# Performance work log

Hardware: AMD Instinct MI355X
Metric: run time of the kernel (lower is better)

## Reference

```python
import jax, jax.numpy as jnp
import numpy as np
from jax import lax

B, T, C, H, W = 2, 5, 2, 128, 256
E, M, L = 64, 16, 4  # embedding_dim, n_fno_modes, n_fno_layers
EPS = 1e-5


def conv1x1(x, w, b):
    # x: [N, I, H, W], w: [O, I], b: [O]
    return jnp.einsum('nihw,oi->nohw', x, w) + b[None, :, None, None]


def conv3x3(x, w, b):
    # x: [N, I, H, W], w: [O, I, 3, 3]
    y = lax.conv_general_dilated(x, w, window_strides=(1, 1), padding='SAME',
                                 dimension_numbers=('NCHW', 'OIHW', 'NCHW'))
    return y + b[None, :, None, None]


def instance_norm(x):
    # InstanceNorm2d(affine=False): normalize over H,W per (n, c), biased var
    mu = jnp.mean(x, axis=(2, 3), keepdims=True)
    var = jnp.var(x, axis=(2, 3), keepdims=True)
    return (x - mu) * lax.rsqrt(var + EPS)


def upsample2x_nearest(x):
    return jnp.repeat(jnp.repeat(x, 2, axis=2), 2, axis=3)


def resize_nearest(x, out_h, out_w):
    # torch F.interpolate mode='nearest': idx = floor(i * in / out)
    in_h, in_w = x.shape[2], x.shape[3]
    hi = (jnp.arange(out_h) * in_h) // out_h
    wi = (jnp.arange(out_w) * in_w) // out_w
    return x[:, :, hi, :][:, :, :, wi]


def fno_layer(x, wr, wi, cw, cb):
    # x: [N, E, H, W]; wr/wi: [2, E, E, M, M]; cw: [E, E]; cb: [E]
    h, w = x.shape[2], x.shape[3]
    coeff = jnp.fft.rfft2(x, axes=(2, 3), norm='ortho')  # [N, E, H, W//2+1]
    w0 = wr[0] + 1j * wi[0]
    w1 = wr[1] + 1j * wi[1]
    out = jnp.zeros_like(coeff)
    out = out.at[:, :, :M, :M].set(
        jnp.einsum('nixy,ioxy->noxy', coeff[:, :, :M, :M], w0))
    out = out.at[:, :, -M:, :M].set(
        jnp.einsum('nixy,ioxy->noxy', coeff[:, :, -M:, :M], w1))
    spec = jnp.fft.irfft2(out, s=(h, w), axes=(2, 3), norm='ortho')
    return jax.nn.gelu(conv1x1(x, cw, cb) + spec, approximate=False)


def setup_inputs() -> dict:
    key = jax.random.key(0)
    ks = jax.random.split(key, 10)
    s = 0.02
    return {
        'sensor_value': jax.random.normal(ks[0], (B, T, C, H, W), jnp.float32),
        'updim_w': 0.3 * jax.random.normal(ks[1], (E, C), jnp.float32),
        'updim_b': jnp.zeros((E,), jnp.float32),
        'smooth_w': 0.04 * jax.random.normal(ks[2], (E, E, 3, 3), jnp.float32),
        'smooth_b': jnp.zeros((E,), jnp.float32),
        'fno_wr': s * jax.random.normal(ks[3], (L, 2, E, E, M, M), jnp.float32),
        'fno_wi': s * jax.random.normal(ks[4], (L, 2, E, E, M, M), jnp.float32),
        'fno_cw': 0.1 * jax.random.normal(ks[5], (L, E, E), jnp.float32),
        'fno_cb': jnp.zeros((L, E), jnp.float32),
        'downdim_w': 0.1 * jax.random.normal(ks[6], (C, E), jnp.float32),
        'downdim_b': jnp.zeros((C,), jnp.float32),
    }


def reference(sensor_value, updim_w, updim_b, smooth_w, smooth_b,
              fno_wr, fno_wi, fno_cw, fno_cb, downdim_w, downdim_b):
    b, t, c, h, w = sensor_value.shape
    x = sensor_value.reshape(b * t, c, h, w)
    x = conv1x1(x, updim_w, updim_b)
    x = upsample2x_nearest(x)
    x = jax.nn.gelu(instance_norm(conv3x3(x, smooth_w, smooth_b)), approximate=False)
    x = resize_nearest(x, H, W)
    for l in range(L):
        x = fno_layer(x, fno_wr[l], fno_wi[l], fno_cw[l], fno_cb[l])
    x = conv1x1(x, downdim_w, downdim_b)
    return x.reshape(b, t, c, H, W)
```

## Files before the change

kernel.cpp:

```cpp
#include <hip/hip_runtime.h>
#include <math.h>

#define PI_D 3.14159265358979323846


typedef _Float16 h8 __attribute__((ext_vector_type(8)));
typedef float f16v __attribute__((ext_vector_type(16)));

__device__ __forceinline__ float gelu_f(float v){
  return 0.5f*v*(1.0f + erff(v*0.70710678118654752440f));
}

__device__ __forceinline__ int fsw_c(int w){ return (w ^ (w >> 3)) & 7; }

__global__ __launch_bounds__(256) void k_tables_fold(float* __restrict__ twFwH, float* __restrict__ twBwH,
                                                     _Float16* __restrict__ Tspec, _Float16* __restrict__ TdftW,
                                                     const float* __restrict__ smw, const float* __restrict__ upw,
                                                     const float* __restrict__ upb, float* __restrict__ Keff){
  int bid = blockIdx.x;
  if (bid < 96){
    int id = bid*256 + threadIdx.x;
    if (id < 4096){
      int h = id >> 5, m = id & 31;
      int xm = (m < 16) ? m : (96 + m);
      double ang = -2.0*PI_D*(double)((xm*h) & 127)/128.0;
      twFwH[id*2]   = (float)cos(ang);
      twFwH[id*2+1] = (float)sin(ang);
    } else if (id < 8192){
      int j = id - 4096;
      int h = j >> 5, m = j & 31;
      int xm = (m < 16) ? m : (96 + m);
      double ang = 2.0*PI_D*(double)((xm*h) & 127)/128.0;
      twBwH[j*2]   = (float)cos(ang);
      twBwH[j*2+1] = (float)sin(ang);
    } else if (id < 16384){
      int j = id - 8192;
      int w = j >> 5, kk = j & 31;
      int y = kk >> 1;
      double ang = 2.0*PI_D*(double)((w*y) & 255)/256.0;
      double v = (kk & 1) ? -sin(ang) : cos(ang);
      Tspec[j] = (_Float16)v;
    } else if (id < 24576){
      int j = id - 16384;
      int y2 = j >> 8, w = j & 255;
      int y = y2 >> 1;
      double ang = -2.0*PI_D*(double)((w*y) & 255)/256.0;
      double v = (y2 & 1) ? sin(ang) : cos(ang);
      TdftW[j] = (_Float16)v;
    }
  } else {
    int id = (bid-96)*256 + threadIdx.x;
    if (id >= 1024) return;
    int o = id >> 4, rs = (id >> 2) & 3, tap = id & 3;
    int r = rs >> 1, s = rs & 1, a = tap >> 1, b = tap & 1;
    int klo = (r==0) ? (a==0?0:1) : (a==0?0:2);
    int khi = (r==0) ? (a==0?0:2) : (a==0?1:2);
    int llo = (s==0) ? (b==0?0:1) : (b==0?0:2);
    int lhi = (s==0) ? (b==0?0:2) : (b==0?1:2);
    float a0=0.f, a1=0.f, ab=0.f;
    for (int i=0;i<64;++i){
      float t = 0.f;
      for (int kh=klo; kh<=khi; ++kh)
        for (int kw=llo; kw<=lhi; ++kw)
          t += smw[((size_t)o*64+i)*9 + kh*3+kw];
      a0 += t*upw[i*2];
      a1 += t*upw[i*2+1];
      ab += t*upb[i];
    }
    *(float4*)(Keff + o*64 + (rs*4+tap)*4) = make_float4(a0, a1, ab, 0.f);
  }
}

__global__ __launch_bounds__(256) void k_transW(const float* __restrict__ wr, const float* __restrict__ wi,
                                                unsigned* __restrict__ Wt){
  __shared__ unsigned P[64*257];
  int lb = blockIdx.x;
  int i = lb & 63, blk = (lb>>6)&1, l = lb>>7;
  int tid = threadIdx.x;
  size_t sbase = (size_t)l*2097152 + (size_t)blk*1048576 + (size_t)i*16384 + tid;
  for (int o=0;o<64;++o){
    float a = wr[sbase + (size_t)o*256];
    float b = wi[sbase + (size_t)o*256];
    union { unsigned u; _Float16 h[2]; } pk;
    pk.h[0] = (_Float16)a; pk.h[1] = (_Float16)b;
    P[o*257 + tid] = pk.u;
  }
  __syncthreads();
  int o = tid & 63, g = tid >> 6;
  size_t dbase = (size_t)(l*2+blk)*1048576;
  for (int it=0; it<64; ++it){
    int my = g*64 + it;
    Wt[dbase + (size_t)my*4096 + i*64 + o] = P[o*257 + my];
  }
}

__global__ __launch_bounds__(512) void k_corrbnd(const float* __restrict__ sv, float* __restrict__ Rpart,
                                                 float* __restrict__ Bnd){
  __shared__ float SH[3120];
  int bid = blockIdx.x;
  int tid = threadIdx.x;
  if (bid < 320){
    int band = bid & 31, n = bid >> 5;
    int u0 = band*4;
    for (int t = tid; t < 3120; t += 512){
      int ch = t / 1560; int rem = t - ch*1560; int rr = rem / 260; int ci = rem - rr*260;
      int row = u0 - 1 + rr, col = ci - 1;
      float v = 0.f;
      if (row >= 0 && row < 128 && col >= 0 && col < 256)
        v = sv[((size_t)(n*2+ch)*128 + row)*256 + col];
      SH[(ch*6+rr)*260 + ci] = v;
    }
    __syncthreads();

    int lane = tid & 63, wv = tid >> 6;
    int c  = (wv<4) ? (wv>>1) : ((wv<6) ? (wv-4) : 2);
    int c2 = (wv<4) ? (wv&1)  : ((wv<6) ? 2 : (wv-6));
    float acc[9];
    #pragma unroll
    for (int k=0;k<9;++k) acc[k]=0.f;

    for (int r=0;r<4;++r){
      int u = u0 + r, lu = r + 1;
      for (int cb=0;cb<4;++cb){
        int v = cb*64 + lane;
        float f = (c==2) ? 1.f : SH[(c*6+lu)*260 + 1+v];
        #pragma unroll
        for (int dr=-1;dr<=1;++dr){
          int ur = u + dr;
          float rko = (ur>=0 && ur<128) ? 1.f : 0.f;
          #pragma unroll
          for (int dc=-1;dc<=1;++dc){
            float g;
            if (c2==2){
              int vc = v + dc;
              g = rko * ((vc>=0 && vc<256) ? 1.f : 0.f);
            } else {
              g = SH[(c2*6+lu+dr)*260 + 1+v+dc];
            }
            acc[(dr+1)*3 + dc+1] += f*g;
          }
        }
      }
    }
    #pragma unroll
    for (int k=0;k<9;++k){
      float v = acc[k];
      for (int off=32; off; off>>=1) v += __shfl_xor(v, off);
      if (lane==0) Rpart[((size_t)(n*32+band)*8 + wv)*9 + k] = v;
    }
  } else {
    int n = bid - 320;
    for (int t = tid; t < 3120; t += 512){
      int e = t/780; int rem = t - e*780; int ch = rem/260; int i = rem - ch*260;
      int idx = i - 1;
      int len = (e<2) ? 256 : 128;
      float v = 0.f;
      if (idx >= 0 && idx < len){
        if (ch==2) v = 1.f;
        else {
          int row = (e==0) ? 0 : (e==1) ? 127 : idx;
          int col = (e==2) ? 0 : (e==3) ? 255 : idx;
          v = sv[((size_t)(n*2+ch)*128 + row)*256 + col];
        }
      }
      SH[(e*3+ch)*260 + i] = v;
    }
    __syncthreads();
    if (tid < 108){
      int e = tid/27; int rem = tid - e*27; int pair = rem/3; int lag = rem%3 - 1;
      int c = pair/3, c2 = pair%3;
      int len = (e<2) ? 256 : 128;
      float a = 0.f;
      for (int i=0;i<len;++i) a += SH[(e*3+c)*260 + 1+i]*SH[(e*3+c2)*260 + 1+i+lag];
      Bnd[n*144 + tid] = a;
    } else if (tid < 144){
      int t = tid - 108; int corner = t/9; int pair = t - corner*9;
      int c = pair/3, c2 = pair%3;
      int e = (corner<2) ? 0 : 1;
      int idx = (corner&1) ? 255 : 0;
      Bnd[n*144 + tid] = SH[(e*3+c)*260 + 1+idx]*SH[(e*3+c2)*260 + 1+idx];
    }
  }
}

__global__ __launch_bounds__(256) void k_stats3(const float* __restrict__ Rpart, const float* __restrict__ Bnd,
                                                const float* __restrict__ Keff, float* __restrict__ stats){
  __shared__ float R[9][9];
  __shared__ float BL[4][9][3];
  __shared__ float CR[4][9];
  __shared__ float M[4][12][12];
  int n = blockIdx.x, tid = threadIdx.x;

  if (tid < 72){
    int wv = tid/9, k = tid - (tid/9)*9;
    double s = 0.0;
    for (int b=0;b<32;++b) s += (double)Rpart[((size_t)(n*32+b)*8 + wv)*9 + k];
    int c  = (wv<4) ? (wv>>1) : ((wv<6) ? (wv-4) : 2);
    int c2 = (wv<4) ? (wv&1)  : ((wv<6) ? 2 : (wv-6));
    R[c*3+c2][k] = (float)s;
  } else if (tid < 81){
    int k = tid - 72; int dr = k/3 - 1, dc = k%3 - 1;
    R[8][k] = (float)((128 - (dr<0?-dr:dr)) * (256 - (dc<0?-dc:dc)));
  }
  if (tid < 108){
    int e = tid/27, rem = tid - (tid/27)*27;
    BL[e][rem/3][rem%3] = Bnd[n*144 + tid];
  } else if (tid < 144){
    int t = tid - 108;
    CR[t/9][t - (t/9)*9] = Bnd[n*144 + tid];
  }
  __syncthreads();

  for (int t = tid; t < 576; t += 256){
    int rs = t/144; int rem = t - rs*144; int i = rem/12, j = rem - (rem/12)*12;
    int ab = i/3,  c  = i - ab*3,  a  = ab>>1, b  = ab&1;
    int ab2 = j/3, c2 = j - ab2*3, a2 = ab2>>1, b2 = ab2&1;
    int r = rs>>1, s = rs&1;
    int dr = a2 - a, dc = b2 - b;
    int pair = c*3 + c2;
    float g = R[pair][(dr+1)*3 + (dc+1)];
    if (r==1 && a==1 && a2==1) g -= BL[0][pair][dc+1];
    if (r==0 && a==0 && a2==0) g -= BL[1][pair][dc+1];
    if (s==1 && b==1 && b2==1) g -= BL[2][pair][dr+1];
    if (s==0 && b==0 && b2==0) g -= BL[3][pair][dr+1];
    bool rowc = (a==a2) && ((r==1 && a==1) || (r==0 && a==0));
    bool colc = (b==b2) && ((s==1 && b==1) || (s==0 && b==0));
    if (rowc && colc){
      int corner = ((r==1)?0:2) + ((s==1)?0:1);
      g += CR[corner][pair];
    }
    M[rs][i][j] = g;
  }
  __syncthreads();

  if (tid < 64){
    int o = tid;
    double S1 = 0.0, S2 = 0.0;
    for (int rs=0; rs<4; ++rs){
      float w[12];
      #pragma unroll
      for (int ab=0; ab<4; ++ab){
        float4 kv = *(const float4*)(Keff + o*64 + (rs*4+ab)*4);
        w[ab*3+0] = kv.x; w[ab*3+1] = kv.y; w[ab*3+2] = kv.z;
      }
      #pragma unroll
      for (int i=0;i<12;++i){
        double ti = 0.0;
        #pragma unroll
        for (int j=0;j<12;++j) ti += (double)M[rs][i][j]*(double)w[j];
        S2 += (double)w[i]*ti;
      }
      #pragma unroll
      for (int ab=0; ab<4; ++ab)
        #pragma unroll
        for (int c=0;c<3;++c)
          S1 += (double)w[ab*3+c]*(double)M[rs][ab*3+c][ab*3+2];
    }
    double mu  = S1 / 131072.0;
    double var = S2 / 131072.0 - mu*mu;
    stats[(n*64+o)*2]   = (float)mu;
    stats[(n*64+o)*2+1] = (float)(1.0/sqrt(var + 1e-5));
  }
}

__global__ __launch_bounds__(256) void k_convnorm(const float* __restrict__ sv,
                                                  const float* __restrict__ Keff,
                                                  const float* __restrict__ stats,
                                                  _Float16* __restrict__ act){
  __shared__ float SV[4*260];
  int bid = blockIdx.x;
  int p = bid & 127, n = bid >> 7;
  int tid = threadIdx.x;
  for (int t = tid; t < 1032; t += 256){
    int dr = t / 516;
    int rem = t - dr*516;
    int ch = rem / 258;
    int ci = rem - ch*258;
    int row = p - 1 + dr;
    int col = ci - 1;
    float v = 0.f;
    if (row >= 0 && col >= 0 && col < 256)
      v = sv[((size_t)(n*2+ch)*128 + row)*256 + col];
    SV[(dr*2+ch)*260 + ci] = v;
  }
  __syncthreads();

  int q = tid;
  float x0[4], x1[4], ib[4];
  float rowok0 = (p>0)?1.f:0.f;
  float colok0 = (q>0)?1.f:0.f;
  #pragma unroll
  for (int a=0;a<2;++a)
    #pragma unroll
    for (int b=0;b<2;++b){
      x0[a*2+b] = SV[(a*2+0)*260 + q + b];
      x1[a*2+b] = SV[(a*2+1)*260 + q + b];
      ib[a*2+b] = (a==0?rowok0:1.f) * (b==0?colok0:1.f);
    }

  for (int o=0; o<64; ++o){
    const float4* kp = (const float4*)(Keff + o*64);
    float y = 0.f;
    #pragma unroll
    for (int t=0;t<4;++t){
      float4 kv = kp[t];
      y += kv.x*x0[t] + kv.y*x1[t] + kv.z*ib[t];
    }
    float mu = stats[(n*64+o)*2], istd = stats[(n*64+o)*2+1];
    float v = (y - mu)*istd;
    act[((size_t)(n*64+o)*128 + p)*256 + q] = (_Float16)gelu_f(v);
  }
}

__global__ __launch_bounds__(256, 2) void k_dftW_mfma(const _Float16* __restrict__ act,
                                                      const _Float16* __restrict__ TdftW,
                                                      float* __restrict__ Cy){
  __shared__ _Float16 Ax[32768];
  __shared__ _Float16 Bt[8192];
  int tid = threadIdx.x;
  int hp = blockIdx.x & 63, n = blockIdx.x >> 6;
  int h0 = hp*2;

  {
    int a = tid >> 1;
    int ws = (tid & 1) * 128;
    int e = a & 63, ht = a >> 6;
    const _Float16* src = act + ((size_t)(n*64+e))*32768 + (size_t)(h0+ht)*256 + ws;
    #pragma unroll
    for (int k=0;k<16;++k){
      h8 v = *(const h8*)(src + k*8);
      int wq = (ws >> 3) + k;
      int chunk = wq ^ (a & 7);
      *(h8*)(Ax + a*256 + chunk*8) = v;
    }
  }
  {
    int y2 = tid & 31, ws = (tid >> 5) * 32;
    const _Float16* src = TdftW + y2*256 + ws;
    #pragma unroll
    for (int k=0;k<4;++k){
      h8 v = *(const h8*)(src + k*8);
      int wq = (ws >> 3) + k;
      int chunk = wq ^ (y2 & 7);
      *(h8*)(Bt + y2*256 + chunk*8) = v;
    }
  }
  __syncthreads();

  int lane = tid & 63;
  int l31 = lane & 31, l5 = lane >> 5;
  int mt = tid >> 6;
  int a = mt*32 + l31;

  f16v acc;
  #pragma unroll
  for (int j=0;j<16;++j) acc[j] = 0.f;
  #pragma unroll
  for (int ks=0;ks<16;++ks){
    int kb = ks*16 + l5*8;
    int cA = (kb>>3) ^ (a & 7);
    int cB = (kb>>3) ^ (l31 & 7);
    h8 af = *(const h8*)(Ax + a*256 + cA*8);
    h8 bf = *(const h8*)(Bt + l31*256 + cB*8);
    acc = __builtin_amdgcn_mfma_f32_32x32x16_f16(bf, af, acc, 0,0,0);
  }
  int e = a & 63, ht = a >> 6;
  #pragma unroll
  for (int j=0;j<16;j+=2){
    int y2 = (j&3) + 8*(j>>2) + 4*l5;
    int yy = y2 >> 1;
    *(float2*)(Cy + (((size_t)(n*16+yy)*128 + h0+ht)*64 + e)*2) = make_float2(acc[j], acc[j+1]);
  }
}

__global__ __launch_bounds__(256) void k_specAB(const float* __restrict__ Cy,
                                                const float* __restrict__ twF,
                                                const unsigned* __restrict__ Wt,
                                                float* __restrict__ MS, int l){
  __shared__ float CO[8*64*2];
  int bid = blockIdx.x;
  int mq = bid / 160;
  int pid = bid - mq*160;
  int y = pid & 15, n = pid >> 4;
  int tid = threadIdx.x;
  int lane = tid & 63;
  int wv = __builtin_amdgcn_readfirstlane(tid >> 6);

  {
    int m0 = mq*8 + wv*2;
    const float* cyb = Cy + (((size_t)(n*16+y)*128)*64 + lane)*2;
    const float* tf = twF + m0*2;
    float ar0=0.f, ai0=0.f, ar1=0.f, ai1=0.f;
    for (int h=0; h<128; ++h){
      float2 c = *(const float2*)(cyb + h*128);
      const float* tp = tf + h*64;
      float t0r = tp[0], t0i = tp[1], t1r = tp[2], t1i = tp[3];
      ar0 += t0r*c.x - t0i*c.y; ai0 += t0r*c.y + t0i*c.x;
      ar1 += t1r*c.x - t1i*c.y; ai1 += t1r*c.y + t1i*c.x;
    }
    int mm = wv*2;
    *(float2*)(CO + (mm*64 + lane)*2)     = make_float2(ar0, ai0);
    *(float2*)(CO + ((mm+1)*64 + lane)*2) = make_float2(ar1, ai1);
  }
  __syncthreads();

  {
    #pragma unroll
    for (int t2=0; t2<2; ++t2){
      int mm = wv*2 + t2;
      int m = mq*8 + mm;
      int blk = m >> 4, mloc = m & 15;
      int my = mloc*16 + y;
      const unsigned* wb = Wt + ((size_t)((l*2+blk)*256 + my))*4096 + lane;
      float mr = 0.f, mi = 0.f;
      for (int i=0;i<64;++i){
        float2 cc = *(const float2*)(CO + (mm*64 + i)*2);
        union { unsigned u; _Float16 h[2]; } pk;
        pk.u = wb[(size_t)i*64];
        float wr_f = (float)pk.h[0], wi_f = (float)pk.h[1];
        mr += cc.x*wr_f - cc.y*wi_f;
        mi += cc.x*wi_f + cc.y*wr_f;
      }
      *(float2*)(MS + (((size_t)(n*16+y)*32 + m)*64 + lane)*2) = make_float2(mr, mi);
    }
  }
}

__global__ __launch_bounds__(256) void k_specC(const float* __restrict__ MS,
                                               const float* __restrict__ twB,
                                               float* __restrict__ G){
  __shared__ float SM[32*64*2];
  int bid = blockIdx.x;
  int hq = bid / 160;
  int pid = bid - hq*160;
  int y = pid & 15, n = pid >> 4;
  int tid = threadIdx.x;
  int lane = tid & 63;
  int wv = __builtin_amdgcn_readfirstlane(tid >> 6);

  {
    const float4* src = (const float4*)(MS + ((size_t)(n*16+y)*32)*128);
    float4* dst = (float4*)SM;
    #pragma unroll
    for (int t=0; t<4; ++t) dst[tid + t*256] = src[tid + t*256];
  }
  __syncthreads();

  float f = (y==0) ? (1.f/32768.f) : (2.f/32768.f);
  for (int k=0;k<8;++k){
    int h = hq*32 + wv*8 + k;
    const float* tb = twB + h*64;
    float gr=0.f, gi=0.f;
    #pragma unroll
    for (int m=0;m<32;++m){
      float tr = tb[m*2], ti = tb[m*2+1];
      float2 mo2 = *(const float2*)(SM + (m*64+lane)*2);
      gr += tr*mo2.x - ti*mo2.y;
      gi += tr*mo2.y + ti*mo2.x;
    }
    size_t gb = (((size_t)(n*128+h)*16 + y)*2)*64 + lane;
    G[gb]      = gr*f;
    G[gb + 64] = gi*f;
  }
}

__global__ __launch_bounds__(512, 4) void k_combine_mfma(const _Float16* __restrict__ act_in,
                                                         const float* __restrict__ G,
                                                         const _Float16* __restrict__ Tspec,
                                                         const _Float16* __restrict__ TdftW,
                                                         const float* __restrict__ cw,
                                                         const float* __restrict__ cb,
                                                         const float* __restrict__ wd,
                                                         const float* __restrict__ bd,
                                                         _Float16* __restrict__ act_out,
                                                         float* __restrict__ Cy,
                                                         float* __restrict__ outp,
                                                         int flags){
  __shared__ __align__(16) _Float16 Lh[40960];
  _Float16* Bx = Lh;
  _Float16* At = Lh + 32768;
  int tid = threadIdx.x;
  int h = blockIdx.x & 127, n = blockIdx.x >> 7;

  {
    int rp = tid >> 4, sub = tid & 15;
    int i0 = 2*rp;
    int wbase = sub*16;
    const _Float16* r0 = act_in + (size_t)(n*64+i0)*32768 + (size_t)h*256 + wbase;
    const _Float16* r1 = r0 + 32768;
    h8 A0 = *(const h8*)r0,     A1 = *(const h8*)(r0+8);
    h8 B0 = *(const h8*)r1,     B1 = *(const h8*)(r1+8);
    int cbs = rp >> 2;
    int lo  = i0 & 7;
    #pragma unroll
    for (int k=0;k<16;++k){
      union { _Float16 hh[2]; unsigned u; } pk;
      pk.hh[0] = (k<8) ? A0[k] : A1[k-8];
      pk.hh[1] = (k<8) ? B0[k] : B1[k-8];
      int w = wbase + k;
      int chunk = cbs ^ fsw_c(w);
      *(unsigned*)(Bx + w*128 + chunk*8 + lo) = pk.u;
    }
  }
  {
    int o = tid >> 3, seg = (tid & 7)*8;
    float4 c0 = *(const float4*)(cw + o*64 + seg);
    float4 c1 = *(const float4*)(cw + o*64 + seg + 4);
    h8 v;
    v[0]=(_Float16)c0.x; v[1]=(_Float16)c0.y; v[2]=(_Float16)c0.z; v[3]=(_Float16)c0.w;
    v[4]=(_Float16)c1.x; v[5]=(_Float16)c1.y; v[6]=(_Float16)c1.z; v[7]=(_Float16)c1.w;
    int ch0 = (seg>>3) ^ (o & 7);
    *(h8*)(At + o*128 + ch0*8) = v;
  }
  {
    const float* gp = G + (size_t)(n*128 + h)*2048 + tid*4;
    float4 g = *(const float4*)gp;
    float gvx[4] = {g.x, g.y, g.z, g.w};
    int idx0 = tid*4;
    int yc = idx0 >> 6;
    int o0 = idx0 & 63;
    int kk = 64 + yc;
    #pragma unroll
    for (int j=0;j<4;++j){
      int o = o0 + j;
      int chunk = (kk >> 3) ^ (o & 7);
      At[o*128 + chunk*8 + (kk & 7)] = (_Float16)gvx[j];
    }
  }
  {
    int w = tid >> 1, half = tid & 1;
    const _Float16* tp = Tspec + w*32 + half*16;
    #pragma unroll
    for (int c=0;c<2;++c){
      h8 v = *(const h8*)(tp + c*8);
      int cc = half*2 + c;
      int chunk = (8 + cc) ^ fsw_c(w);
      *(h8*)(Bx + w*128 + chunk*8) = v;
    }
  }
  __syncthreads();

  int lane = tid & 63;
  int l31 = lane & 31, l5 = lane >> 5;
  int w0i = tid >> 6;
  int mt = w0i & 1, ng = w0i >> 1;
  int o_lane = mt*32 + l31;

  h8 af[6];
  #pragma unroll
  for (int ks=0;ks<6;++ks){
    int kb = ks*16 + l5*8;
    int chunk = (kb>>3) ^ (o_lane & 7);
    af[ks] = *(const h8*)(At + o_lane*128 + chunk*8);
  }
  float bias[16];
  #pragma unroll
  for (int j=0;j<16;++j) bias[j] = cb[mt*32 + (j&3) + 8*(j>>2) + 4*l5];

  f16v acc[2];
  #pragma unroll
  for (int q=0;q<2;++q)
    #pragma unroll
    for (int j=0;j<16;++j) acc[q][j] = bias[j];

  #pragma unroll
  for (int q=0;q<2;++q){
    int w = (ng*2+q)*32 + l31;
    const _Float16* bbase = Bx + w*128;
    int wf = fsw_c(w);
    #pragma unroll
    for (int ks=0;ks<6;++ks){
      int kb = ks*16 + l5*8;
      int chunk = (kb>>3) ^ wf;
      h8 bf = *(const h8*)(bbase + chunk*8);
      acc[q] = __builtin_amdgcn_mfma_f32_32x32x16_f16(af[ks], bf, acc[q], 0,0,0);
    }
  }

  float gvv[32];
  #pragma unroll
  for (int q=0;q<2;++q)
    #pragma unroll
    for (int j=0;j<16;++j) gvv[q*16+j] = gelu_f(acc[q][j]);

  if (flags != 2){
    #pragma unroll
    for (int q=0;q<2;++q){
      int wcol = (ng*2+q)*32 + l31;
      #pragma unroll
      for (int j=0;j<16;++j){
        int o = mt*32 + (j&3) + 8*(j>>2) + 4*l5;
        act_out[(size_t)(n*64+o)*32768 + (size_t)h*256 + wcol] = (_Float16)gvv[q*16+j];
      }
    }
  }
  __syncthreads();

  if (flags == 1){
    _Float16* gL  = Lh;
    _Float16* TdL = Lh + 16384;
    #pragma unroll
    for (int q=0;q<2;++q){
      int wcol = (ng*2+q)*32 + l31;
      int wc3 = wcol >> 3, wc7 = wcol & 7;
      #pragma unroll
      for (int j=0;j<16;++j){
        int o = mt*32 + (j&3) + 8*(j>>2) + 4*l5;
        gL[o*256 + ((wc3 ^ (o & 7))*8) + wc7] = (_Float16)gvv[q*16+j];
      }
    }
    {
      int y2 = tid & 31, ws = (tid >> 5)*16;
      const _Float16* src = TdftW + y2*256 + ws;
      #pragma unroll
      for (int k=0;k<2;++k){
        h8 v = *(const h8*)(src + k*8);
        int chunk = ((ws>>3)+k) ^ (y2 & 7);
        *(h8*)(TdL + y2*256 + chunk*8) = v;
      }
    }
    __syncthreads();
    float* P = (float*)(Lh + 32768);
    if (w0i < 4){
      int mt2 = w0i & 1, kh = w0i >> 1;
      int ocol = mt2*32 + l31;
      f16v acc2;
      #pragma unroll
      for (int j=0;j<16;++j) acc2[j] = 0.f;
      #pragma unroll
      for (int ks=0;ks<8;++ks){
        int kb = (kh*8+ks)*16 + l5*8;
        h8 af2 = *(const h8*)(gL  + ocol*256 + (((kb>>3) ^ (ocol & 7))*8));
        h8 bf2 = *(const h8*)(TdL + l31*256  + (((kb>>3) ^ (l31 & 7))*8));
        acc2 = __builtin_amdgcn_mfma_f32_32x32x16_f16(bf2, af2, acc2, 0,0,0);
      }
      #pragma unroll
      for (int j=0;j<16;++j){
        int y2 = (j&3) + 8*(j>>2) + 4*l5;
        P[w0i*1024 + y2*32 + l31] = acc2[j];
      }
    }
    __syncthreads();
    #pragma unroll
    for (int rep=0;rep<2;++rep){
      int t = rep*512 + tid;
      int yy = t >> 6, o = t & 63, mt2 = o >> 5, o31 = o & 31;
      float re = P[mt2*1024 + (2*yy)*32 + o31]   + P[(2+mt2)*1024 + (2*yy)*32 + o31];
      float im = P[mt2*1024 + (2*yy+1)*32 + o31] + P[(2+mt2)*1024 + (2*yy+1)*32 + o31];
      *(float2*)(Cy + (((size_t)(n*16+yy)*128 + h)*64 + o)*2) = make_float2(re, im);
    }
  } else {
    float p00=0.f,p01=0.f,p10=0.f,p11=0.f;
    #pragma unroll
    for (int j=0;j<16;++j){
      int o = mt*32 + (j&3) + 8*(j>>2) + 4*l5;
      float w0d = wd[o], w1d = wd[64+o];
      p00 += w0d*gvv[j];     p10 += w1d*gvv[j];
      p01 += w0d*gvv[16+j];  p11 += w1d*gvv[16+j];
    }
    p00 += __shfl_xor(p00,32); p10 += __shfl_xor(p10,32);
    p01 += __shfl_xor(p01,32); p11 += __shfl_xor(p11,32);
    float* red = (float*)(Lh + 32768);
    if (l5 == 0){
      int wa = (ng*2+0)*32 + l31, wb2 = (ng*2+1)*32 + l31;
      red[wa*4  + mt*2 + 0] = p00; red[wa*4  + mt*2 + 1] = p10;
      red[wb2*4 + mt*2 + 0] = p01; red[wb2*4 + mt*2 + 1] = p11;
    }
    __syncthreads();
    {
      int ch = tid >> 8, wcol = tid & 255;
      float v = red[wcol*4 + ch] + red[wcol*4 + 2 + ch] + bd[ch];
      outp[(size_t)n*65536 + (size_t)ch*32768 + (size_t)h*256 + wcol] = v;
    }
  }
}

extern "C" void kernel_launch(void* const* d_in, const int* in_sizes, int n_in,
                              void* d_out, int out_size, void* d_ws, size_t ws_size,
                              hipStream_t stream) {
  const float* sv  = (const float*)d_in[0];
  const float* upw = (const float*)d_in[1];
  const float* upb = (const float*)d_in[2];
  const float* smw = (const float*)d_in[3];
  const float* smb = (const float*)d_in[4];
  const float* fwr = (const float*)d_in[5];
  const float* fwi = (const float*)d_in[6];
  const float* fcw = (const float*)d_in[7];
  const float* fcb = (const float*)d_in[8];
  const float* ddw = (const float*)d_in[9];
  const float* ddb = (const float*)d_in[10];
  float* out = (float*)d_out;
  (void)smb;

  float* W = (float*)d_ws;
  _Float16* actA = (_Float16*)W;
  _Float16* actB = (_Float16*)(W + 10485760);
  float* Cy    = W + 20971520;
  float* G     = W + 23592960;
  float* part  = W + 26214400;
  float* stats = W + 28180480;
  float* Keff  = W + 28181760;
  float* twFwH = W + 28185856;
  float* twBwH = W + 28194048;
  _Float16* Tspec = (_Float16*)(W + 28202240);
  _Float16* TdftW = (_Float16*)(W + 28206336);
  unsigned* Wt   = (unsigned*)(W + 28210432);

  float* Rpart = part;
  float* Bnd   = part + 30000;
  float* MS    = part + 65536;

  k_tables_fold<<<100,256,0,stream>>>(twFwH, twBwH, Tspec, TdftW, smw, upw, upb, Keff);
  k_transW<<<512,256,0,stream>>>(fwr, fwi, Wt);
  k_corrbnd<<<330,512,0,stream>>>(sv, Rpart, Bnd);
  k_stats3<<<10,256,0,stream>>>(Rpart, Bnd, Keff, stats);
  k_convnorm<<<1280,256,0,stream>>>(sv, Keff, stats, actA);
  k_dftW_mfma<<<640,256,0,stream>>>(actA, TdftW, Cy);

  _Float16* xa = actA; _Float16* xb = actB;
  for (int l=0;l<4;++l){
    k_specAB<<<640,256,0,stream>>>(Cy, twFwH, Wt, MS, l);
    k_specC<<<640,256,0,stream>>>(MS, twBwH, G);
    k_combine_mfma<<<1280,512,0,stream>>>(xa, G, Tspec, TdftW,
                                          fcw + (size_t)l*4096, fcb + (size_t)l*64,
                                          ddw, ddb, xb, Cy, out, (l<3)?1:2);
    _Float16* t = xa; xa = xb; xb = t;
  }
}
```

Before: 460.7 us.

## Double combine kernel block size to 1024 threads, one MFMA tile per wave

The combine kernel now launches 1024 threads per block instead of 512, so each wave computes a single 32x32 output tile rather than two, and the load and reduction phases are redistributed across the extra threads (the G load goes to the upper half, and the DFT reduction is split four ways over eight waves). The aim is more waves in flight per block, with lower register pressure per thread, to hide memory and MFMA latency. In exchange it adds more per-block barrier overhead and a larger partial-sum reduction in LDS. The launch-bounds hint of 8 blocks per CU may also be unachievable given LDS and register use.

```diff
diff --git a/kernel.cpp b/kernel.cpp
--- a/kernel.cpp
+++ b/kernel.cpp
@@ -464,18 +464,18 @@
   }
 }
 
-__global__ __launch_bounds__(512, 4) void k_combine_mfma(const _Float16* __restrict__ act_in,
-                                                         const float* __restrict__ G,
-                                                         const _Float16* __restrict__ Tspec,
-                                                         const _Float16* __restrict__ TdftW,
-                                                         const float* __restrict__ cw,
-                                                         const float* __restrict__ cb,
-                                                         const float* __restrict__ wd,
-                                                         const float* __restrict__ bd,
-                                                         _Float16* __restrict__ act_out,
-                                                         float* __restrict__ Cy,
-                                                         float* __restrict__ outp,
-                                                         int flags){
+__global__ __launch_bounds__(1024, 8) void k_combine_mfma(const _Float16* __restrict__ act_in,
+                                                          const float* __restrict__ G,
+                                                          const _Float16* __restrict__ Tspec,
+                                                          const _Float16* __restrict__ TdftW,
+                                                          const float* __restrict__ cw,
+                                                          const float* __restrict__ cb,
+                                                          const float* __restrict__ wd,
+                                                          const float* __restrict__ bd,
+                                                          _Float16* __restrict__ act_out,
+                                                          float* __restrict__ Cy,
+                                                          float* __restrict__ outp,
+                                                          int flags){
   __shared__ __align__(16) _Float16 Lh[40960];
   _Float16* Bx = Lh;
   _Float16* At = Lh + 32768;
@@ -483,26 +483,26 @@
   int h = blockIdx.x & 127, n = blockIdx.x >> 7;
 
   {
-    int rp = tid >> 4, sub = tid & 15;
+    int rp = tid >> 5, sub = tid & 31;
     int i0 = 2*rp;
-    int wbase = sub*16;
+    int wbase = sub*8;
     const _Float16* r0 = act_in + (size_t)(n*64+i0)*32768 + (size_t)h*256 + wbase;
     const _Float16* r1 = r0 + 32768;
-    h8 A0 = *(const h8*)r0,     A1 = *(const h8*)(r0+8);
-    h8 B0 = *(const h8*)r1,     B1 = *(const h8*)(r1+8);
+    h8 A0 = *(const h8*)r0;
+    h8 B0 = *(const h8*)r1;
     int cbs = rp >> 2;
     int lo  = i0 & 7;
     #pragma unroll
-    for (int k=0;k<16;++k){
+    for (int k=0;k<8;++k){
       union { _Float16 hh[2]; unsigned u; } pk;
-      pk.hh[0] = (k<8) ? A0[k] : A1[k-8];
-      pk.hh[1] = (k<8) ? B0[k] : B1[k-8];
+      pk.hh[0] = A0[k];
+      pk.hh[1] = B0[k];
       int w = wbase + k;
       int chunk = cbs ^ fsw_c(w);
       *(unsigned*)(Bx + w*128 + chunk*8 + lo) = pk.u;
     }
   }
-  {
+  if (tid < 512){
     int o = tid >> 3, seg = (tid & 7)*8;
     float4 c0 = *(const float4*)(cw + o*64 + seg);
     float4 c1 = *(const float4*)(cw + o*64 + seg + 4);
@@ -511,12 +511,12 @@
     v[4]=(_Float16)c1.x; v[5]=(_Float16)c1.y; v[6]=(_Float16)c1.z; v[7]=(_Float16)c1.w;
     int ch0 = (seg>>3) ^ (o & 7);
     *(h8*)(At + o*128 + ch0*8) = v;
-  }
-  {
-    const float* gp = G + (size_t)(n*128 + h)*2048 + tid*4;
+  } else {
+    int t5 = tid - 512;
+    const float* gp = G + (size_t)(n*128 + h)*2048 + t5*4;
     float4 g = *(const float4*)gp;
     float gvx[4] = {g.x, g.y, g.z, g.w};
-    int idx0 = tid*4;
+    int idx0 = t5*4;
     int yc = idx0 >> 6;
     int o0 = idx0 & 63;
     int kk = 64 + yc;
@@ -527,7 +527,7 @@
       At[o*128 + chunk*8 + (kk & 7)] = (_Float16)gvx[j];
     }
   }
-  {
+  if (tid < 512){
     int w = tid >> 1, half = tid & 1;
     const _Float16* tp = Tspec + w*32 + half*16;
     #pragma unroll
@@ -553,19 +553,13 @@
     int chunk = (kb>>3) ^ (o_lane & 7);
     af[ks] = *(const h8*)(At + o_lane*128 + chunk*8);
   }
-  float bias[16];
+
+  f16v acc;
   #pragma unroll
-  for (int j=0;j<16;++j) bias[j] = cb[mt*32 + (j&3) + 8*(j>>2) + 4*l5];
-
-  f16v acc[2];
-  #pragma unroll
-  for (int q=0;q<2;++q)
-    #pragma unroll
-    for (int j=0;j<16;++j) acc[q][j] = bias[j];
-
-  #pragma unroll
-  for (int q=0;q<2;++q){
-    int w = (ng*2+q)*32 + l31;
+  for (int j=0;j<16;++j) acc[j] = cb[mt*32 + (j&3) + 8*(j>>2) + 4*l5];
+
+  {
+    int w = ng*32 + l31;
     const _Float16* bbase = Bx + w*128;
     int wf = fsw_c(w);
     #pragma unroll
@@ -573,25 +567,20 @@
       int kb = ks*16 + l5*8;
       int chunk = (kb>>3) ^ wf;
       h8 bf = *(const h8*)(bbase + chunk*8);
-      acc[q] = __builtin_amdgcn_mfma_f32_32x32x16_f16(af[ks], bf, acc[q], 0,0,0);
-    }
-  }
-
-  float gvv[32];
+      acc = __builtin_amdgcn_mfma_f32_32x32x16_f16(af[ks], bf, acc, 0,0,0);
+    }
+  }
+
+  float gvv[16];
   #pragma unroll
-  for (int q=0;q<2;++q)
-    #pragma unroll
-    for (int j=0;j<16;++j) gvv[q*16+j] = gelu_f(acc[q][j]);
-
+  for (int j=0;j<16;++j) gvv[j] = gelu_f(acc[j]);
+
+  int wcol = ng*32 + l31;
   if (flags != 2){
     #pragma unroll
-    for (int q=0;q<2;++q){
-      int wcol = (ng*2+q)*32 + l31;
-      #pragma unroll
-      for (int j=0;j<16;++j){
-        int o = mt*32 + (j&3) + 8*(j>>2) + 4*l5;
-        act_out[(size_t)(n*64+o)*32768 + (size_t)h*256 + wcol] = (_Float16)gvv[q*16+j];
-      }
+    for (int j=0;j<16;++j){
+      int o = mt*32 + (j&3) + 8*(j>>2) + 4*l5;
+      act_out[(size_t)(n*64+o)*32768 + (size_t)h*256 + wcol] = (_Float16)gvv[j];
     }
   }
   __syncthreads();
@@ -599,37 +588,32 @@
   if (flags == 1){
     _Float16* gL  = Lh;
     _Float16* TdL = Lh + 16384;
-    #pragma unroll
-    for (int q=0;q<2;++q){
-      int wcol = (ng*2+q)*32 + l31;
+    {
       int wc3 = wcol >> 3, wc7 = wcol & 7;
       #pragma unroll
       for (int j=0;j<16;++j){
         int o = mt*32 + (j&3) + 8*(j>>2) + 4*l5;
-        gL[o*256 + ((wc3 ^ (o & 7))*8) + wc7] = (_Float16)gvv[q*16+j];
+        gL[o*256 + ((wc3 ^ (o & 7))*8) + wc7] = (_Float16)gvv[j];
       }
     }
     {
-      int y2 = tid & 31, ws = (tid >> 5)*16;
+      int y2 = tid & 31, ws = (tid >> 5)*8;
       const _Float16* src = TdftW + y2*256 + ws;
-      #pragma unroll
-      for (int k=0;k<2;++k){
-        h8 v = *(const h8*)(src + k*8);
-        int chunk = ((ws>>3)+k) ^ (y2 & 7);
-        *(h8*)(TdL + y2*256 + chunk*8) = v;
-      }
+      h8 v = *(const h8*)src;
+      int chunk = (ws>>3) ^ (y2 & 7);
+      *(h8*)(TdL + y2*256 + chunk*8) = v;
     }
     __syncthreads();
-    float* P = (float*)(Lh + 32768);
-    if (w0i < 4){
-      int mt2 = w0i & 1, kh = w0i >> 1;
+    float* P = (float*)(Lh + 24576);
+    if (w0i < 8){
+      int mt2 = w0i & 1, kq = w0i >> 1;
       int ocol = mt2*32 + l31;
       f16v acc2;
       #pragma unroll
       for (int j=0;j<16;++j) acc2[j] = 0.f;
       #pragma unroll
-      for (int ks=0;ks<8;++ks){
-        int kb = (kh*8+ks)*16 + l5*8;
+      for (int ks=0;ks<4;++ks){
+        int kb = (kq*4+ks)*16 + l5*8;
         h8 af2 = *(const h8*)(gL  + ocol*256 + (((kb>>3) ^ (ocol & 7))*8));
         h8 bf2 = *(const h8*)(TdL + l31*256  + (((kb>>3) ^ (l31 & 7))*8));
         acc2 = __builtin_amdgcn_mfma_f32_32x32x16_f16(bf2, af2, acc2, 0,0,0);
@@ -641,36 +625,34 @@
       }
     }
     __syncthreads();
-    #pragma unroll
-    for (int rep=0;rep<2;++rep){
-      int t = rep*512 + tid;
-      int yy = t >> 6, o = t & 63, mt2 = o >> 5, o31 = o & 31;
-      float re = P[mt2*1024 + (2*yy)*32 + o31]   + P[(2+mt2)*1024 + (2*yy)*32 + o31];
-      float im = P[mt2*1024 + (2*yy+1)*32 + o31] + P[(2+mt2)*1024 + (2*yy+1)*32 + o31];
+    {
+      int yy = tid >> 6, o = tid & 63, mt2 = o >> 5, o31 = o & 31;
+      float re = P[(0*2+mt2)*1024 + (2*yy)*32 + o31]   + P[(1*2+mt2)*1024 + (2*yy)*32 + o31]
+               + P[(2*2+mt2)*1024 + (2*yy)*32 + o31]   + P[(3*2+mt2)*1024 + (2*yy)*32 + o31];
+      float im = P[(0*2+mt2)*1024 + (2*yy+1)*32 + o31] + P[(1*2+mt2)*1024 + (2*yy+1)*32 + o31]
+               + P[(2*2+mt2)*1024 + (2*yy+1)*32 + o31] + P[(3*2+mt2)*1024 + (2*yy+1)*32 + o31];
       *(float2*)(Cy + (((size_t)(n*16+yy)*128 + h)*64 + o)*2) = make_float2(re, im);
     }
   } else {
-    float p00=0.f,p01=0.f,p10=0.f,p11=0.f;
+    float p0=0.f, p1=0.f;
     #pragma unroll
     for (int j=0;j<16;++j){
       int o = mt*32 + (j&3) + 8*(j>>2) + 4*l5;
-      float w0d = wd[o], w1d = wd[64+o];
-      p00 += w0d*gvv[j];     p10 += w1d*gvv[j];
-      p01 += w0d*gvv[16+j];  p11 += w1d*gvv[16+j];
-    }
-    p00 += __shfl_xor(p00,32); p10 += __shfl_xor(p10,32);
-    p01 += __shfl_xor(p01,32); p11 += __shfl_xor(p11,32);
+      p0 += wd[o]*gvv[j];
+      p1 += wd[64+o]*gvv[j];
+    }
+    p0 += __shfl_xor(p0,32);
+    p1 += __shfl_xor(p1,32);
     float* red = (float*)(Lh + 32768);
     if (l5 == 0){
-      int wa = (ng*2+0)*32 + l31, wb2 = (ng*2+1)*32 + l31;
-      red[wa*4  + mt*2 + 0] = p00; red[wa*4  + mt*2 + 1] = p10;
-      red[wb2*4 + mt*2 + 0] = p01; red[wb2*4 + mt*2 + 1] = p11;
+      red[wcol*4 + mt*2 + 0] = p0;
+      red[wcol*4 + mt*2 + 1] = p1;
     }
     __syncthreads();
-    {
-      int ch = tid >> 8, wcol = tid & 255;
-      float v = red[wcol*4 + ch] + red[wcol*4 + 2 + ch] + bd[ch];
-      outp[(size_t)n*65536 + (size_t)ch*32768 + (size_t)h*256 + wcol] = v;
+    if (tid < 512){
+      int ch = tid >> 8, wc = tid & 255;
+      float v = red[wc*4 + ch] + red[wc*4 + 2 + ch] + bd[ch];
+      outp[(size_t)n*65536 + (size_t)ch*32768 + (size_t)h*256 + wc] = v;
     }
   }
 }
@@ -721,9 +703,9 @@
   for (int l=0;l<4;++l){
     k_specAB<<<640,256,0,stream>>>(Cy, twFwH, Wt, MS, l);
     k_specC<<<640,256,0,stream>>>(MS, twBwH, G);
-    k_combine_mfma<<<1280,512,0,stream>>>(xa, G, Tspec, TdftW,
-                                          fcw + (size_t)l*4096, fcb + (size_t)l*64,
-                                          ddw, ddb, xb, Cy, out, (l<3)?1:2);
+    k_combine_mfma<<<1280,1024,0,stream>>>(xa, G, Tspec, TdftW,
+                                           fcw + (size_t)l*4096, fcb + (size_t)l*64,
+                                           ddw, ddb, xb, Cy, out, (l<3)?1:2);
     _Float16* t = xa; xa = xb; xb = t;
   }
 }
```

Result: no change. 466.7 us (+1.3%).

## Fuse first-layer W-direction DFT into conv-norm kernel via shared memory

Applied to the files above, without the earlier changes.

The conv+instance-norm+GELU kernel now keeps each output row of activations in swizzled LDS and runs the W-direction DFT MFMA in the same block, writing Cy directly. This removes the separate k_dftW_mfma launch and its re-read of the full fp16 activation tensor from global memory. The block doubles to 512 threads, with two output-channel groups and a split-K MFMA reduction through LDS. Only 4 of 8 waves do the MFMA work, and the larger LDS footprint per block may cut occupancy.

```diff
diff --git a/kernel.cpp b/kernel.cpp
--- a/kernel.cpp
+++ b/kernel.cpp
@@ -263,15 +263,21 @@
   }
 }
 
-__global__ __launch_bounds__(256) void k_convnorm(const float* __restrict__ sv,
-                                                  const float* __restrict__ Keff,
-                                                  const float* __restrict__ stats,
-                                                  _Float16* __restrict__ act){
-  __shared__ float SV[4*260];
+__global__ __launch_bounds__(512, 4) void k_convnorm(const float* __restrict__ sv,
+                                                     const float* __restrict__ Keff,
+                                                     const float* __restrict__ stats,
+                                                     const _Float16* __restrict__ TdftW,
+                                                     _Float16* __restrict__ act,
+                                                     float* __restrict__ Cy){
+  __shared__ __align__(16) _Float16 Lh[32768];
+  _Float16* gL  = Lh;
+  _Float16* TdL = Lh + 16384;
+  float*    P   = (float*)(Lh + 24576);
+  float*    SV  = P;
   int bid = blockIdx.x;
   int p = bid & 127, n = bid >> 7;
   int tid = threadIdx.x;
-  for (int t = tid; t < 1032; t += 256){
+  for (int t = tid; t < 1032; t += 512){
     int dr = t / 516;
     int rem = t - dr*516;
     int ch = rem / 258;
@@ -283,9 +289,20 @@
       v = sv[((size_t)(n*2+ch)*128 + row)*256 + col];
     SV[(dr*2+ch)*260 + ci] = v;
   }
-  __syncthreads();
-
-  int q = tid;
+  {
+    int y2 = tid & 31, ws = (tid >> 5)*16;
+    const _Float16* src = TdftW + y2*256 + ws;
+    #pragma unroll
+    for (int k=0;k<2;++k){
+      h8 v = *(const h8*)(src + k*8);
+      int chunk = ((ws>>3)+k) ^ (y2 & 7);
+      *(h8*)(TdL + y2*256 + chunk*8) = v;
+    }
+  }
+  __syncthreads();
+
+  int q = tid & 255;
+  int og = tid >> 8;
   float x0[4], x1[4], ib[4];
   float rowok0 = (p>0)?1.f:0.f;
   float colok0 = (q>0)?1.f:0.f;
@@ -298,7 +315,10 @@
       ib[a*2+b] = (a==0?rowok0:1.f) * (b==0?colok0:1.f);
     }
 
-  for (int o=0; o<64; ++o){
+  int q3 = q>>3, q7 = q&7;
+  #pragma unroll
+  for (int oi=0; oi<32; ++oi){
+    int o = og*32 + oi;
     const float4* kp = (const float4*)(Keff + o*64);
     float y = 0.f;
     #pragma unroll
@@ -307,69 +327,42 @@
       y += kv.x*x0[t] + kv.y*x1[t] + kv.z*ib[t];
     }
     float mu = stats[(n*64+o)*2], istd = stats[(n*64+o)*2+1];
-    float v = (y - mu)*istd;
-    act[((size_t)(n*64+o)*128 + p)*256 + q] = (_Float16)gelu_f(v);
-  }
-}
-
-__global__ __launch_bounds__(256, 2) void k_dftW_mfma(const _Float16* __restrict__ act,
-                                                      const _Float16* __restrict__ TdftW,
-                                                      float* __restrict__ Cy){
-  __shared__ _Float16 Ax[32768];
-  __shared__ _Float16 Bt[8192];
-  int tid = threadIdx.x;
-  int hp = blockIdx.x & 63, n = blockIdx.x >> 6;
-  int h0 = hp*2;
-
-  {
-    int a = tid >> 1;
-    int ws = (tid & 1) * 128;
-    int e = a & 63, ht = a >> 6;
-    const _Float16* src = act + ((size_t)(n*64+e))*32768 + (size_t)(h0+ht)*256 + ws;
-    #pragma unroll
-    for (int k=0;k<16;++k){
-      h8 v = *(const h8*)(src + k*8);
-      int wq = (ws >> 3) + k;
-      int chunk = wq ^ (a & 7);
-      *(h8*)(Ax + a*256 + chunk*8) = v;
-    }
-  }
-  {
-    int y2 = tid & 31, ws = (tid >> 5) * 32;
-    const _Float16* src = TdftW + y2*256 + ws;
-    #pragma unroll
-    for (int k=0;k<4;++k){
-      h8 v = *(const h8*)(src + k*8);
-      int wq = (ws >> 3) + k;
-      int chunk = wq ^ (y2 & 7);
-      *(h8*)(Bt + y2*256 + chunk*8) = v;
-    }
+    _Float16 gh = (_Float16)gelu_f((y - mu)*istd);
+    gL[o*256 + ((q3 ^ (o & 7))*8) + q7] = gh;
+    act[((size_t)(n*64+o)*128 + p)*256 + q] = gh;
   }
   __syncthreads();
 
   int lane = tid & 63;
   int l31 = lane & 31, l5 = lane >> 5;
-  int mt = tid >> 6;
-  int a = mt*32 + l31;
-
-  f16v acc;
+  int w0i = tid >> 6;
+  if (w0i < 4){
+    int mt2 = w0i & 1, kh = w0i >> 1;
+    int ocol = mt2*32 + l31;
+    f16v acc2;
+    #pragma unroll
+    for (int j=0;j<16;++j) acc2[j] = 0.f;
+    #pragma unroll
+    for (int ks=0;ks<8;++ks){
+      int kb = (kh*8+ks)*16 + l5*8;
+      h8 af2 = *(const h8*)(gL  + ocol*256 + (((kb>>3) ^ (ocol & 7))*8));
+      h8 bf2 = *(const h8*)(TdL + l31*256  + (((kb>>3) ^ (l31 & 7))*8));
+      acc2 = __builtin_amdgcn_mfma_f32_32x32x16_f16(bf2, af2, acc2, 0,0,0);
+    }
+    #pragma unroll
+    for (int j=0;j<16;++j){
+      int y2 = (j&3) + 8*(j>>2) + 4*l5;
+      P[w0i*1024 + y2*32 + l31] = acc2[j];
+    }
+  }
+  __syncthreads();
   #pragma unroll
-  for (int j=0;j<16;++j) acc[j] = 0.f;
-  #pragma unroll
-  for (int ks=0;ks<16;++ks){
-    int kb = ks*16 + l5*8;
-    int cA = (kb>>3) ^ (a & 7);
-    int cB = (kb>>3) ^ (l31 & 7);
-    h8 af = *(const h8*)(Ax + a*256 + cA*8);
-    h8 bf = *(const h8*)(Bt + l31*256 + cB*8);
-    acc = __builtin_amdgcn_mfma_f32_32x32x16_f16(bf, af, acc, 0,0,0);
-  }
-  int e = a & 63, ht = a >> 6;
-  #pragma unroll
-  for (int j=0;j<16;j+=2){
-    int y2 = (j&3) + 8*(j>>2) + 4*l5;
-    int yy = y2 >> 1;
-    *(float2*)(Cy + (((size_t)(n*16+yy)*128 + h0+ht)*64 + e)*2) = make_float2(acc[j], acc[j+1]);
+  for (int rep=0;rep<2;++rep){
+    int t = rep*512 + tid;
+    int yy = t >> 6, o = t & 63, mt2 = o >> 5, o31 = o & 31;
+    float re = P[mt2*1024 + (2*yy)*32 + o31]   + P[(2+mt2)*1024 + (2*yy)*32 + o31];
+    float im = P[mt2*1024 + (2*yy+1)*32 + o31] + P[(2+mt2)*1024 + (2*yy+1)*32 + o31];
+    *(float2*)(Cy + (((size_t)(n*16+yy)*128 + p)*64 + o)*2) = make_float2(re, im);
   }
 }
 
@@ -714,8 +707,7 @@
   k_transW<<<512,256,0,stream>>>(fwr, fwi, Wt);
   k_corrbnd<<<330,512,0,stream>>>(sv, Rpart, Bnd);
   k_stats3<<<10,256,0,stream>>>(Rpart, Bnd, Keff, stats);
-  k_convnorm<<<1280,256,0,stream>>>(sv, Keff, stats, actA);
-  k_dftW_mfma<<<640,256,0,stream>>>(actA, TdftW, Cy);
+  k_convnorm<<<1280,512,0,stream>>>(sv, Keff, stats, TdftW, actA, Cy);
 
   _Float16* xa = actA; _Float16* xb = actB;
   for (int l=0;l<4;++l){
```

Result: slower. 474.0 us (+2.9%).
